# Performance work log

Measured on AMD Instinct MI355X. Metric: run time of the kernel, lower is better.

Reference implementation:

```python
import jax, jax.numpy as jnp
import numpy as np

B, N, F = 4, 4096, 64

def setup_inputs() -> dict:
    key = jax.random.key(0)
    ks = jax.random.split(key, 7)
    X = jax.random.normal(ks[0], (B, N, F), dtype=jnp.float32)
    A0 = jax.random.uniform(ks[1], (B, N, N), dtype=jnp.float32)
    A1 = jax.random.uniform(ks[2], (B, N, N), dtype=jnp.float32)
    A2 = jax.random.uniform(ks[3], (B, N, N), dtype=jnp.float32)
    w0 = jax.random.normal(ks[4], (F, F), dtype=jnp.float32) * 0.05
    w1 = jax.random.normal(ks[5], (F, F), dtype=jnp.float32) * 0.05
    w2 = jax.random.normal(ks[6], (F, F), dtype=jnp.float32) * 0.05
    return {"X": X, "A0": A0, "A1": A1, "A2": A2, "w0": w0, "w1": w1, "w2": w2}

def reference(X, A0, A1, A2, w0, w1, w2):
    # Three parallel (A @ X) @ W chains, summed, then ReLU.
    # bnm,bmf->bnf then bnf,fg->bng
    p0 = jnp.einsum('bnf,fg->bng', jnp.matmul(A0, X), w0)
    p1 = jnp.einsum('bnf,fg->bng', jnp.matmul(A1, X), w1)
    p2 = jnp.einsum('bnf,fg->bng', jnp.matmul(A2, X), w2)
    return jax.nn.relu(p0 + p1 + p2)
```

## Files before the change

### kernel.cpp

```cpp
#include <hip/hip_runtime.h>

#define NN 4096
#define BB 4
#define FF 64

typedef __attribute__((ext_vector_type(8))) short short8;
typedef __attribute__((ext_vector_type(4))) float f32x4;

__device__ inline unsigned short f2bf(float f) {
    unsigned int u = __float_as_uint(f);
    u += 0x7fffu + ((u >> 16) & 1u);
    return (unsigned short)(u >> 16);
}

__global__ __launch_bounds__(256) void prep_z(
    const float* __restrict__ X,
    const float* __restrict__ w0, const float* __restrict__ w1, const float* __restrict__ w2,
    unsigned short* __restrict__ Zt)
{
    __shared__ float Xs[64][68];
    __shared__ unsigned short Zts[64][72];
    const int blk = blockIdx.x;
    const int b = blk >> 6;
    const int k0 = (blk & 63) << 6;
    const int t = threadIdx.x;
    {
        const int kk = t >> 2, c4 = t & 3;
        const float* src = X + ((size_t)b * NN + k0 + kk) * FF;
        #pragma unroll
        for (int p = 0; p < 4; ++p) {
            float4 v = *(const float4*)(src + 4 * (c4 + 4 * p));
            *(float4*)&Xs[kk][4 * (c4 + 4 * p)] = v;
        }
    }
    __syncthreads();
    const int lane = t & 63, w = t >> 6;
    const float* ws[3] = {w0, w1, w2};
    for (int i = 0; i < 3; ++i) {
        float acc[16];
        #pragma unroll
        for (int j = 0; j < 16; ++j) acc[j] = 0.f;
        const float* wp = ws[i];
        for (int c = 0; c < 64; ++c) {
            float wv = wp[c * FF + lane];
            #pragma unroll
            for (int j = 0; j < 16; ++j) acc[j] += Xs[w * 16 + j][c] * wv;
        }
        __syncthreads();
        #pragma unroll
        for (int j = 0; j < 16; ++j) Zts[lane][w * 16 + j] = f2bf(acc[j]);
        __syncthreads();
        #pragma unroll
        for (int cc = 0; cc < 2; ++cc) {
            int ch = t + cc * 256;
            int f = ch >> 3, o8 = (ch & 7) * 8;
            float4 v = *(const float4*)&Zts[f][o8];
            *(float4*)(Zt + (((size_t)i * BB + b) * FF + f) * NN + k0 + o8) = v;
        }
    }
}

__global__ __launch_bounds__(768) void gnn_main(
    const float* __restrict__ A0, const float* __restrict__ A1, const float* __restrict__ A2,
    const unsigned short* __restrict__ Zt,
    float* __restrict__ out)
{
    __shared__ unsigned short lds[3 * 2 * 64 * 72];
    const int blk = blockIdx.x;
    const int b = blk >> 6;
    const int m0 = (blk & 63) << 6;
    const int t = threadIdx.x;
    const int lane = t & 63;
    const int wave = t >> 6;
    const int ig = wave >> 2;
    const int w4 = wave & 3;
    const int gtid = t & 255;

    const float* Ai = (ig == 0) ? A0 : (ig == 1) ? A1 : A2;
    unsigned short* As = lds + ig * (2 * 64 * 72);
    unsigned short* Zs = As + 64 * 72;

    const int r = gtid >> 2, c4 = gtid & 3;
    const float* Abase = Ai + (size_t)b * NN * NN + (size_t)(m0 + r) * NN;
    const int zf0 = gtid >> 3, zo0 = (gtid & 7) * 8;
    const int zf1 = (gtid + 256) >> 3, zo1 = ((gtid + 256) & 7) * 8;
    const unsigned short* Zbase = Zt + (((size_t)ig * BB + b) * FF) * NN;
    const unsigned short* Zp0 = Zbase + (size_t)zf0 * NN + zo0;
    const unsigned short* Zp1 = Zbase + (size_t)zf1 * NN + zo1;

    f32x4 acc[4] = {};

    float4 apf[4];
    float4 zpf0, zpf1;
    #pragma unroll
    for (int p = 0; p < 4; ++p) apf[p] = *(const float4*)(Abase + 4 * c4 + 16 * p);
    zpf0 = *(const float4*)Zp0;
    zpf1 = *(const float4*)Zp1;

    const unsigned short* Arow = As + (w4 * 16 + (lane & 15)) * 72 + (lane >> 4) * 8;
    const unsigned short* Zrow = Zs + (lane & 15) * 72 + (lane >> 4) * 8;

    for (int step = 0; step < 64; ++step) {
        __syncthreads();
        #pragma unroll
        for (int p = 0; p < 4; ++p) {
            ushort4 u;
            u.x = f2bf(apf[p].x); u.y = f2bf(apf[p].y);
            u.z = f2bf(apf[p].z); u.w = f2bf(apf[p].w);
            *(ushort4*)(As + r * 72 + 4 * c4 + 16 * p) = u;
        }
        *(float4*)(Zs + zf0 * 72 + zo0) = zpf0;
        *(float4*)(Zs + zf1 * 72 + zo1) = zpf1;
        if (step < 63) {
            const float* Ab = Abase + (step + 1) * 64;
            #pragma unroll
            for (int p = 0; p < 4; ++p) apf[p] = *(const float4*)(Ab + 4 * c4 + 16 * p);
            zpf0 = *(const float4*)(Zp0 + (step + 1) * 64);
            zpf1 = *(const float4*)(Zp1 + (step + 1) * 64);
        }
        __syncthreads();
        #pragma unroll
        for (int kh = 0; kh < 2; ++kh) {
            short8 af = *(const short8*)(Arow + kh * 32);
            #pragma unroll
            for (int nt = 0; nt < 4; ++nt) {
                short8 bf = *(const short8*)(Zrow + nt * 16 * 72 + kh * 32);
                acc[nt] = __builtin_amdgcn_mfma_f32_16x16x32_bf16(af, bf, acc[nt], 0, 0, 0);
            }
        }
    }

    __syncthreads();
    float* Cred = (float*)lds;
    for (int g = 0; g < 3; ++g) {
        if (ig == g) {
            #pragma unroll
            for (int nt = 0; nt < 4; ++nt) {
                #pragma unroll
                for (int j = 0; j < 4; ++j) {
                    int row = w4 * 16 + (lane >> 4) * 4 + j;
                    int col = nt * 16 + (lane & 15);
                    if (g == 0) Cred[row * 68 + col] = acc[nt][j];
                    else        Cred[row * 68 + col] += acc[nt][j];
                }
            }
        }
        __syncthreads();
    }
    if (ig == 0) {
        float* orow = out + ((size_t)b * NN + m0 + r) * FF;
        #pragma unroll
        for (int p = 0; p < 4; ++p) {
            int c0 = 4 * (c4 + 4 * p);
            float4 v = *(const float4*)&Cred[r * 68 + c0];
            v.x = fmaxf(v.x, 0.f); v.y = fmaxf(v.y, 0.f);
            v.z = fmaxf(v.z, 0.f); v.w = fmaxf(v.w, 0.f);
            *(float4*)(orow + c0) = v;
        }
    }
}

extern "C" void kernel_launch(void* const* d_in, const int* in_sizes, int n_in,
                              void* d_out, int out_size, void* d_ws, size_t ws_size,
                              hipStream_t stream) {
    const float* X  = (const float*)d_in[0];
    const float* A0 = (const float*)d_in[1];
    const float* A1 = (const float*)d_in[2];
    const float* A2 = (const float*)d_in[3];
    const float* w0 = (const float*)d_in[4];
    const float* w1 = (const float*)d_in[5];
    const float* w2 = (const float*)d_in[6];
    float* out = (float*)d_out;
    unsigned short* Zt = (unsigned short*)d_ws;

    prep_z<<<256, 256, 0, stream>>>(X, w0, w1, w2, Zt);
    gnn_main<<<256, 768, 0, stream>>>(A0, A1, A2, Zt, out);
}
```

Baseline: 751.3 us.

## Stream A and Z directly into registers with split-K waves, dropping LDS staging

The main kernel stops staging A and Z tiles through shared memory. Each wave loads its MFMA operands straight from global memory into registers, double-buffered across K halves, and splits K in two across wave pairs. The block tile shrinks to 32 rows, giving 512 blocks with a block swizzle, and partial sums are reduced in LDS at the end. The prep kernel fuses the three weight products into one pass. The aim is to remove the per-step barriers and LDS traffic and to raise occupancy and memory-level parallelism. In exchange, Z is reloaded from global memory by more blocks and the per-lane access patterns are less coalesced.

Result: no change. 740.5 us (-1.4%).

```diff
diff --git a/kernel.cpp b/kernel.cpp
--- a/kernel.cpp
+++ b/kernel.cpp
@@ -13,150 +13,184 @@
     return (unsigned short)(u >> 16);
 }
 
-__global__ __launch_bounds__(256) void prep_z(
+__device__ inline short8 cvt8(float4 lo, float4 hi) {
+    short8 r;
+    r[0] = (short)f2bf(lo.x); r[1] = (short)f2bf(lo.y);
+    r[2] = (short)f2bf(lo.z); r[3] = (short)f2bf(lo.w);
+    r[4] = (short)f2bf(hi.x); r[5] = (short)f2bf(hi.y);
+    r[6] = (short)f2bf(hi.z); r[7] = (short)f2bf(hi.w);
+    return r;
+}
+
+__global__ __launch_bounds__(512) void prep_z(
     const float* __restrict__ X,
     const float* __restrict__ w0, const float* __restrict__ w1, const float* __restrict__ w2,
     unsigned short* __restrict__ Zt)
 {
     __shared__ float Xs[64][68];
-    __shared__ unsigned short Zts[64][72];
     const int blk = blockIdx.x;
     const int b = blk >> 6;
     const int k0 = (blk & 63) << 6;
     const int t = threadIdx.x;
     {
-        const int kk = t >> 2, c4 = t & 3;
-        const float* src = X + ((size_t)b * NN + k0 + kk) * FF;
-        #pragma unroll
-        for (int p = 0; p < 4; ++p) {
-            float4 v = *(const float4*)(src + 4 * (c4 + 4 * p));
-            *(float4*)&Xs[kk][4 * (c4 + 4 * p)] = v;
+        const int kk = t >> 3, c8 = (t & 7) * 8;
+        const float* src = X + ((size_t)(b * NN + k0 + kk)) * FF + c8;
+        *(float4*)&Xs[kk][c8]     = *(const float4*)(src);
+        *(float4*)&Xs[kk][c8 + 4] = *(const float4*)(src + 4);
+    }
+    __syncthreads();
+    const int lane = t & 63;
+    const int w = t >> 6;
+    float acc0[8] = {}, acc1[8] = {}, acc2[8] = {};
+    #pragma unroll 2
+    for (int c4 = 0; c4 < 16; ++c4) {
+        float4 xv[8];
+        #pragma unroll
+        for (int j = 0; j < 8; ++j) xv[j] = *(const float4*)&Xs[w * 8 + j][c4 * 4];
+        #pragma unroll
+        for (int cc = 0; cc < 4; ++cc) {
+            const int c = c4 * 4 + cc;
+            const float wv0 = w0[c * FF + lane];
+            const float wv1 = w1[c * FF + lane];
+            const float wv2 = w2[c * FF + lane];
+            #pragma unroll
+            for (int j = 0; j < 8; ++j) {
+                const float x = ((const float*)&xv[j])[cc];
+                acc0[j] = fmaf(x, wv0, acc0[j]);
+                acc1[j] = fmaf(x, wv1, acc1[j]);
+                acc2[j] = fmaf(x, wv2, acc2[j]);
+            }
         }
     }
-    __syncthreads();
-    const int lane = t & 63, w = t >> 6;
-    const float* ws[3] = {w0, w1, w2};
-    for (int i = 0; i < 3; ++i) {
-        float acc[16];
-        #pragma unroll
-        for (int j = 0; j < 16; ++j) acc[j] = 0.f;
-        const float* wp = ws[i];
-        for (int c = 0; c < 64; ++c) {
-            float wv = wp[c * FF + lane];
-            #pragma unroll
-            for (int j = 0; j < 16; ++j) acc[j] += Xs[w * 16 + j][c] * wv;
-        }
-        __syncthreads();
-        #pragma unroll
-        for (int j = 0; j < 16; ++j) Zts[lane][w * 16 + j] = f2bf(acc[j]);
-        __syncthreads();
-        #pragma unroll
-        for (int cc = 0; cc < 2; ++cc) {
-            int ch = t + cc * 256;
-            int f = ch >> 3, o8 = (ch & 7) * 8;
-            float4 v = *(const float4*)&Zts[f][o8];
-            *(float4*)(Zt + (((size_t)i * BB + b) * FF + f) * NN + k0 + o8) = v;
-        }
-    }
-}
-
-__global__ __launch_bounds__(768) void gnn_main(
+    unsigned short* zp = Zt + ((size_t)(b * FF + lane)) * NN + k0 + w * 8;
+    const size_t plane = (size_t)BB * FF * NN;
+    {
+        short8 v;
+        #pragma unroll
+        for (int e = 0; e < 8; ++e) v[e] = (short)f2bf(acc0[e]);
+        *(short8*)zp = v;
+    }
+    zp += plane;
+    {
+        short8 v;
+        #pragma unroll
+        for (int e = 0; e < 8; ++e) v[e] = (short)f2bf(acc1[e]);
+        *(short8*)zp = v;
+    }
+    zp += plane;
+    {
+        short8 v;
+        #pragma unroll
+        for (int e = 0; e < 8; ++e) v[e] = (short)f2bf(acc2[e]);
+        *(short8*)zp = v;
+    }
+}
+
+#define MFMA8(AF0, AF1, Z0, Z1, Z2, Z3)                                                   \
+    acc[0][0] = __builtin_amdgcn_mfma_f32_16x16x32_bf16(AF0, Z0, acc[0][0], 0, 0, 0);     \
+    acc[0][1] = __builtin_amdgcn_mfma_f32_16x16x32_bf16(AF0, Z1, acc[0][1], 0, 0, 0);     \
+    acc[0][2] = __builtin_amdgcn_mfma_f32_16x16x32_bf16(AF0, Z2, acc[0][2], 0, 0, 0);     \
+    acc[0][3] = __builtin_amdgcn_mfma_f32_16x16x32_bf16(AF0, Z3, acc[0][3], 0, 0, 0);     \
+    acc[1][0] = __builtin_amdgcn_mfma_f32_16x16x32_bf16(AF1, Z0, acc[1][0], 0, 0, 0);     \
+    acc[1][1] = __builtin_amdgcn_mfma_f32_16x16x32_bf16(AF1, Z1, acc[1][1], 0, 0, 0);     \
+    acc[1][2] = __builtin_amdgcn_mfma_f32_16x16x32_bf16(AF1, Z2, acc[1][2], 0, 0, 0);     \
+    acc[1][3] = __builtin_amdgcn_mfma_f32_16x16x32_bf16(AF1, Z3, acc[1][3], 0, 0, 0);
+
+__global__ __launch_bounds__(384, 3) void gnn_main(
     const float* __restrict__ A0, const float* __restrict__ A1, const float* __restrict__ A2,
     const unsigned short* __restrict__ Zt,
     float* __restrict__ out)
 {
-    __shared__ unsigned short lds[3 * 2 * 64 * 72];
-    const int blk = blockIdx.x;
-    const int b = blk >> 6;
-    const int m0 = (blk & 63) << 6;
+    __shared__ float red[2][32][68];
+    const int nb = (int)blockIdx.x;
+    const int swz = (nb & 7) * 64 + (nb >> 3);
+    const int b  = swz >> 7;
+    const int m0 = (swz & 127) << 5;
     const int t = threadIdx.x;
     const int lane = t & 63;
     const int wave = t >> 6;
-    const int ig = wave >> 2;
-    const int w4 = wave & 3;
-    const int gtid = t & 255;
+    const int ig = wave >> 1;
+    const int kh = wave & 1;
+    const int r = lane & 15;
+    const int g = lane >> 4;
 
     const float* Ai = (ig == 0) ? A0 : (ig == 1) ? A1 : A2;
-    unsigned short* As = lds + ig * (2 * 64 * 72);
-    unsigned short* Zs = As + 64 * 72;
-
-    const int r = gtid >> 2, c4 = gtid & 3;
-    const float* Abase = Ai + (size_t)b * NN * NN + (size_t)(m0 + r) * NN;
-    const int zf0 = gtid >> 3, zo0 = (gtid & 7) * 8;
-    const int zf1 = (gtid + 256) >> 3, zo1 = ((gtid + 256) & 7) * 8;
-    const unsigned short* Zbase = Zt + (((size_t)ig * BB + b) * FF) * NN;
-    const unsigned short* Zp0 = Zbase + (size_t)zf0 * NN + zo0;
-    const unsigned short* Zp1 = Zbase + (size_t)zf1 * NN + zo1;
-
-    f32x4 acc[4] = {};
-
-    float4 apf[4];
-    float4 zpf0, zpf1;
+    const float* pA0 = Ai + ((size_t)(b * NN + m0 + r)) * NN + kh * 2048 + g * 8;
+    const float* pA1 = pA0 + (size_t)16 * NN;
+    const unsigned short* pZ0 =
+        Zt + ((size_t)((ig * BB + b) * FF + r)) * NN + kh * 2048 + g * 8;
+    const unsigned short* pZ1 = pZ0 + (size_t)16 * NN;
+    const unsigned short* pZ2 = pZ0 + (size_t)32 * NN;
+    const unsigned short* pZ3 = pZ0 + (size_t)48 * NN;
+
+    f32x4 acc[2][4] = {};
+
+    float4 a00 = *(const float4*)(pA0);      float4 a01 = *(const float4*)(pA0 + 4);
+    float4 a10 = *(const float4*)(pA1);      float4 a11 = *(const float4*)(pA1 + 4);
+    short8 z00 = *(const short8*)(pZ0);      short8 z01 = *(const short8*)(pZ1);
+    short8 z02 = *(const short8*)(pZ2);      short8 z03 = *(const short8*)(pZ3);
+    float4 b00 = *(const float4*)(pA0 + 32); float4 b01 = *(const float4*)(pA0 + 36);
+    float4 b10 = *(const float4*)(pA1 + 32); float4 b11 = *(const float4*)(pA1 + 36);
+    short8 z10 = *(const short8*)(pZ0 + 32); short8 z11 = *(const short8*)(pZ1 + 32);
+    short8 z12 = *(const short8*)(pZ2 + 32); short8 z13 = *(const short8*)(pZ3 + 32);
+    pA0 += 64; pA1 += 64; pZ0 += 64; pZ1 += 64; pZ2 += 64; pZ3 += 64;
+
+    for (int it = 0; it < 62; it += 2) {
+        short8 af0 = cvt8(a00, a01);
+        short8 af1 = cvt8(a10, a11);
+        a00 = *(const float4*)(pA0);      a01 = *(const float4*)(pA0 + 4);
+        a10 = *(const float4*)(pA1);      a11 = *(const float4*)(pA1 + 4);
+        MFMA8(af0, af1, z00, z01, z02, z03)
+        z00 = *(const short8*)(pZ0);      z01 = *(const short8*)(pZ1);
+        z02 = *(const short8*)(pZ2);      z03 = *(const short8*)(pZ3);
+
+        af0 = cvt8(b00, b01);
+        af1 = cvt8(b10, b11);
+        b00 = *(const float4*)(pA0 + 32); b01 = *(const float4*)(pA0 + 36);
+        b10 = *(const float4*)(pA1 + 32); b11 = *(const float4*)(pA1 + 36);
+        MFMA8(af0, af1, z10, z11, z12, z13)
+        z10 = *(const short8*)(pZ0 + 32); z11 = *(const short8*)(pZ1 + 32);
+        z12 = *(const short8*)(pZ2 + 32); z13 = *(const short8*)(pZ3 + 32);
+
+        pA0 += 64; pA1 += 64; pZ0 += 64; pZ1 += 64; pZ2 += 64; pZ3 += 64;
+    }
+    {
+        short8 af0 = cvt8(a00, a01);
+        short8 af1 = cvt8(a10, a11);
+        MFMA8(af0, af1, z00, z01, z02, z03)
+        af0 = cvt8(b00, b01);
+        af1 = cvt8(b10, b11);
+        MFMA8(af0, af1, z10, z11, z12, z13)
+    }
+
+    float* buf = &red[kh][0][0];
     #pragma unroll
-    for (int p = 0; p < 4; ++p) apf[p] = *(const float4*)(Abase + 4 * c4 + 16 * p);
-    zpf0 = *(const float4*)Zp0;
-    zpf1 = *(const float4*)Zp1;
-
-    const unsigned short* Arow = As + (w4 * 16 + (lane & 15)) * 72 + (lane >> 4) * 8;
-    const unsigned short* Zrow = Zs + (lane & 15) * 72 + (lane >> 4) * 8;
-
-    for (int step = 0; step < 64; ++step) {
-        __syncthreads();
-        #pragma unroll
-        for (int p = 0; p < 4; ++p) {
-            ushort4 u;
-            u.x = f2bf(apf[p].x); u.y = f2bf(apf[p].y);
-            u.z = f2bf(apf[p].z); u.w = f2bf(apf[p].w);
-            *(ushort4*)(As + r * 72 + 4 * c4 + 16 * p) = u;
-        }
-        *(float4*)(Zs + zf0 * 72 + zo0) = zpf0;
-        *(float4*)(Zs + zf1 * 72 + zo1) = zpf1;
-        if (step < 63) {
-            const float* Ab = Abase + (step + 1) * 64;
+    for (int gph = 0; gph < 3; ++gph) {
+        if (ig == gph) {
             #pragma unroll
-            for (int p = 0; p < 4; ++p) apf[p] = *(const float4*)(Ab + 4 * c4 + 16 * p);
-            zpf0 = *(const float4*)(Zp0 + (step + 1) * 64);
-            zpf1 = *(const float4*)(Zp1 + (step + 1) * 64);
+            for (int mf = 0; mf < 2; ++mf)
+                #pragma unroll
+                for (int nt = 0; nt < 4; ++nt)
+                    #pragma unroll
+                    for (int j = 0; j < 4; ++j) {
+                        const int row = mf * 16 + g * 4 + j;
+                        const int col = nt * 16 + r;
+                        if (gph == 0) buf[row * 68 + col]  = acc[mf][nt][j];
+                        else          buf[row * 68 + col] += acc[mf][nt][j];
+                    }
         }
         __syncthreads();
-        #pragma unroll
-        for (int kh = 0; kh < 2; ++kh) {
-            short8 af = *(const short8*)(Arow + kh * 32);
-            #pragma unroll
-            for (int nt = 0; nt < 4; ++nt) {
-                short8 bf = *(const short8*)(Zrow + nt * 16 * 72 + kh * 32);
-                acc[nt] = __builtin_amdgcn_mfma_f32_16x16x32_bf16(af, bf, acc[nt], 0, 0, 0);
-            }
-        }
-    }
-
-    __syncthreads();
-    float* Cred = (float*)lds;
-    for (int g = 0; g < 3; ++g) {
-        if (ig == g) {
-            #pragma unroll
-            for (int nt = 0; nt < 4; ++nt) {
-                #pragma unroll
-                for (int j = 0; j < 4; ++j) {
-                    int row = w4 * 16 + (lane >> 4) * 4 + j;
-                    int col = nt * 16 + (lane & 15);
-                    if (g == 0) Cred[row * 68 + col] = acc[nt][j];
-                    else        Cred[row * 68 + col] += acc[nt][j];
-                }
-            }
-        }
-        __syncthreads();
-    }
-    if (ig == 0) {
-        float* orow = out + ((size_t)b * NN + m0 + r) * FF;
-        #pragma unroll
-        for (int p = 0; p < 4; ++p) {
-            int c0 = 4 * (c4 + 4 * p);
-            float4 v = *(const float4*)&Cred[r * 68 + c0];
-            v.x = fmaxf(v.x, 0.f); v.y = fmaxf(v.y, 0.f);
-            v.z = fmaxf(v.z, 0.f); v.w = fmaxf(v.w, 0.f);
-            *(float4*)(orow + c0) = v;
-        }
+    }
+    for (int ch = t; ch < 512; ch += 384) {
+        const int row = ch >> 4, c0 = (ch & 15) << 2;
+        const float4 v0 = *(const float4*)&red[0][row][c0];
+        const float4 v1 = *(const float4*)&red[1][row][c0];
+        float4 v;
+        v.x = fmaxf(v0.x + v1.x, 0.f);
+        v.y = fmaxf(v0.y + v1.y, 0.f);
+        v.z = fmaxf(v0.z + v1.z, 0.f);
+        v.w = fmaxf(v0.w + v1.w, 0.f);
+        *(float4*)(out + ((size_t)(b * NN + m0 + row)) * FF + c0) = v;
     }
 }
 
@@ -173,6 +207,6 @@
     float* out = (float*)d_out;
     unsigned short* Zt = (unsigned short*)d_ws;
 
-    prep_z<<<256, 256, 0, stream>>>(X, w0, w1, w2, Zt);
-    gnn_main<<<256, 768, 0, stream>>>(A0, A1, A2, Zt, out);
-}
+    prep_z<<<256, 512, 0, stream>>>(X, w0, w1, w2, Zt);
+    gnn_main<<<512, 384, 0, stream>>>(A0, A1, A2, Zt, out);
+}
```
